# Kernel tuning notes

Hardware: AMD Instinct MI355X
Metric: run time of the kernel (lower is better)

The kernel has to match this reference:

```python
import jax, jax.numpy as jnp
import numpy as np

N, E, F, H, C = 50000, 800000, 128, 256, 40
BN_EPS = 1e-5


def setup_inputs() -> dict:
    key = jax.random.key(0)
    ks = jax.random.split(key, 18)

    def lin(kw, kb, fan_in, fan_out):
        s = 1.0 / np.sqrt(fan_in)
        W = jax.random.uniform(kw, (fan_in, fan_out), minval=-s, maxval=s, dtype=jnp.float32)
        b = jax.random.uniform(kb, (fan_out,), minval=-s, maxval=s, dtype=jnp.float32)
        return W, b

    x = jax.random.normal(ks[0], (N, F), dtype=jnp.float32)
    edge_index = jax.random.randint(ks[1], (2, E), 0, N, dtype=jnp.int32)
    edge_weight = jax.random.uniform(ks[2], (E,), dtype=jnp.float32)

    W_edge, b_edge = lin(ks[3], ks[4], N, H)   # SparseLinear: weight [num_nodes, H]
    W_node, b_node = lin(ks[5], ks[6], F, H)   # node_mlp (single layer)
    W_c1, b_c1 = lin(ks[7], ks[8], H, H)       # cat_lin1
    W_c2, b_c2 = lin(ks[9], ks[10], H, H)      # cat_lin2
    W_f1, b_f1 = lin(ks[11], ks[12], H, H)     # final_mlp layer 1
    W_f2, b_f2 = lin(ks[13], ks[14], H, C)     # final_mlp layer 2 (plain last)
    gamma = jnp.ones((H,), jnp.float32)        # BatchNorm1d weight
    beta = jnp.zeros((H,), jnp.float32)        # BatchNorm1d bias

    return {"x": x, "edge_index": edge_index, "edge_weight": edge_weight,
            "W_edge": W_edge, "b_edge": b_edge, "W_node": W_node, "b_node": b_node,
            "W_c1": W_c1, "b_c1": b_c1, "W_c2": W_c2, "b_c2": b_c2,
            "W_f1": W_f1, "b_f1": b_f1, "gamma": gamma, "beta": beta,
            "W_f2": W_f2, "b_f2": b_f2}


def reference(x, edge_index, edge_weight, W_edge, b_edge, W_node, b_node,
              W_c1, b_c1, W_c2, b_c2, W_f1, b_f1, gamma, beta, W_f2, b_f2):
    src, dst = edge_index[0], edge_index[1]
    # SparseLinear: gather weight rows at sources, scale by edge weight, scatter-add at targets
    msgs = edge_weight[:, None] * W_edge[src]                 # [E, H]
    h_a = jax.ops.segment_sum(msgs, dst, num_segments=W_edge.shape[0]) + b_edge  # [N, H]

    out = h_a + (h_a @ W_c1 + b_c1)
    h_x = x @ W_node + b_node                                  # node_mlp (plain linear)
    out = out + h_x + (h_x @ W_c2 + b_c2)
    out = jax.nn.relu(out)

    # final_mlp: Linear -> ReLU (act_first) -> BatchNorm (training stats) -> Linear
    h = jax.nn.relu(out @ W_f1 + b_f1)
    mu = jnp.mean(h, axis=0)
    var = jnp.mean(jnp.square(h - mu), axis=0)                 # biased var, as torch BN
    h = (h - mu) * jax.lax.rsqrt(var + BN_EPS) * gamma + beta
    return h @ W_f2 + b_f2                                     # [N, C]
```

## Files before the change

### kernel.cpp

```cpp
#include <hip/hip_runtime.h>

#define NN 50000
#define EE 800000
#define FF 128
#define HH 256
#define CC 40
#define BN_EPS 1e-5f
#define NBUCK 196
#define CHK 3200
#define BCAP 6144

typedef float f4 __attribute__((ext_vector_type(4)));
typedef float f2 __attribute__((ext_vector_type(2)));
typedef _Float16 h8 __attribute__((ext_vector_type(8)));
typedef _Float16 h4 __attribute__((ext_vector_type(4)));

#define OFF_NODE 0
#define OFF_C1   32768
#define OFF_F1   98304
#define PW_HALVES 163840

#define SWZ(row, c2) ((c2) ^ (((row) & 7) << 4))

__global__ __launch_bounds__(256)
void k_wcomb(const float* __restrict__ Wn, const float* __restrict__ Wc2,
             float* __restrict__ Wcomb, int* __restrict__ btail,
             float* __restrict__ stats) {
    if (blockIdx.x == 8) {
        if (threadIdx.x < NBUCK) btail[threadIdx.x] = threadIdx.x * BCAP;
        stats[threadIdx.x] = 0.f;
        stats[256 + threadIdx.x] = 0.f;
        return;
    }
    __shared__ float WnL[16][256];
    const int c = threadIdx.x;
    const int r0 = blockIdx.x * 16;
    for (int i = threadIdx.x; i < 16 * 256; i += 256)
        WnL[i >> 8][i & 255] = Wn[(r0 + (i >> 8)) * HH + (i & 255)];
    __syncthreads();
    float acc[16];
#pragma unroll
    for (int r = 0; r < 16; ++r) acc[r] = WnL[r][c];
    for (int k = 0; k < 256; ++k) {
        float wv = Wc2[k * HH + c];
#pragma unroll
        for (int r = 0; r < 16; ++r) acc[r] += WnL[r][k] * wv;
    }
#pragma unroll
    for (int r = 0; r < 16; ++r) Wcomb[(r0 + r) * HH + c] = acc[r];
}

__global__ __launch_bounds__(256)
void k_prep(const float* __restrict__ W, unsigned char* __restrict__ W8,
            const float* __restrict__ x, _Float16* __restrict__ x16) {
    const int gsz = gridDim.x * blockDim.x;
    const int i0 = blockIdx.x * blockDim.x + threadIdx.x;
    for (int j = i0; j < NN * HH / 8; j += gsz) {
        f4 v0 = ((const f4*)W)[j * 2];
        f4 v1 = ((const f4*)W)[j * 2 + 1];
        int p0 = 0, p1 = 0;
        p0 = __builtin_amdgcn_cvt_pk_fp8_f32(v0[0] * 256.f, v0[1] * 256.f, p0, false);
        p0 = __builtin_amdgcn_cvt_pk_fp8_f32(v0[2] * 256.f, v0[3] * 256.f, p0, true);
        p1 = __builtin_amdgcn_cvt_pk_fp8_f32(v1[0] * 256.f, v1[1] * 256.f, p1, false);
        p1 = __builtin_amdgcn_cvt_pk_fp8_f32(v1[2] * 256.f, v1[3] * 256.f, p1, true);
        uint2 u;
        u.x = (unsigned int)p0;
        u.y = (unsigned int)p1;
        ((uint2*)W8)[j] = u;
    }
    for (int j = i0; j < NN * FF / 8; j += gsz) {
        f4 v0 = ((const f4*)x)[j * 2];
        f4 v1 = ((const f4*)x)[j * 2 + 1];
        h8 h;
        h[0] = (_Float16)v0[0]; h[1] = (_Float16)v0[1];
        h[2] = (_Float16)v0[2]; h[3] = (_Float16)v0[3];
        h[4] = (_Float16)v1[0]; h[5] = (_Float16)v1[1];
        h[6] = (_Float16)v1[2]; h[7] = (_Float16)v1[3];
        ((h8*)x16)[j] = h;
    }
}

__global__ __launch_bounds__(256)
void k_pack(const float* __restrict__ Wcomb, const float* __restrict__ W_c1,
            const float* __restrict__ W_c2, const float* __restrict__ W_f1,
            const float* __restrict__ b_node, const float* __restrict__ b_c1,
            const float* __restrict__ b_c2, _Float16* __restrict__ pW,
            float* __restrict__ bB) {
    const int tid = threadIdx.x;
    if (blockIdx.x == 80) {
        int c = tid;
        if (c < HH) {
            float a = 0.f;
            for (int k = 0; k < HH; ++k) a += b_node[k] * W_c2[k * HH + c];
            bB[c] = a + b_node[c] + b_c1[c] + b_c2[c];
        }
        return;
    }
    const int unit = blockIdx.x * 4 + (tid >> 6);
    const int lane = tid & 63, lm = lane & 15, lg = lane >> 4;
    const float* Ws;
    bool addI;
    int u = unit;
    if (u < 64)       { Ws = Wcomb; addI = false; }
    else if (u < 192) { Ws = W_c1;  addI = true;  u -= 64; }
    else              { Ws = W_f1;  addI = false; u -= 192; }
    const int kb = u >> 4, nb = u & 15;
    h8 hv;
#pragma unroll
    for (int j = 0; j < 8; ++j) {
        int kr = kb * 32 + lg * 8 + j;
        int col = nb * 16 + lm;
        float v = Ws[kr * HH + col];
        if (addI && kr == col) v += 1.f;
        hv[j] = (_Float16)v;
    }
    *(h8*)(pW + (size_t)unit * 512 + lane * 8) = hv;
}

__global__ __launch_bounds__(256)
void k_binA(const int* __restrict__ ei, const float* __restrict__ ew,
            int* __restrict__ btail, uint2* __restrict__ tmp) {
    __shared__ int lcnt[NBUCK], lpre[NBUCK], lbase[NBUCK], lcnt2[NBUCK];
    __shared__ int t[256];
    __shared__ uint2 staged[CHK];
    __shared__ unsigned char bslot[CHK];
    const int tid = threadIdx.x;
    const int e0 = blockIdx.x * CHK;
    const int n = min(CHK, EE - e0);
    for (int i = tid; i < NBUCK; i += 256) { lcnt[i] = 0; lcnt2[i] = 0; }
    __syncthreads();
    for (int i = tid; i < n; i += 256) {
        int d = ei[EE + e0 + i];
        atomicAdd(&lcnt[d >> 8], 1);
    }
    __syncthreads();
    {
        int v = (tid < NBUCK) ? lcnt[tid] : 0;
        t[tid] = v;
        __syncthreads();
#pragma unroll
        for (int off = 1; off < 256; off <<= 1) {
            int u = (tid >= off) ? t[tid - off] : 0;
            __syncthreads();
            t[tid] += u;
            __syncthreads();
        }
        if (tid < NBUCK) lpre[tid] = t[tid] - v;
    }
    __syncthreads();
    if (tid < NBUCK && lcnt[tid] > 0)
        lbase[tid] = atomicAdd(&btail[tid], lcnt[tid]);
    __syncthreads();
    for (int i = tid; i < n; i += 256) {
        int e = e0 + i;
        int d = ei[EE + e];
        int b = d >> 8;
        _Float16 hw = (_Float16)ew[e];
        unsigned short hwb = *(unsigned short*)&hw;
        unsigned int lo = (unsigned int)ei[e] | ((unsigned int)hwb << 16);
        int slot = lpre[b] + atomicAdd(&lcnt2[b], 1);
        uint2 v;
        v.x = lo;
        v.y = (unsigned int)d;
        staged[slot] = v;
        bslot[slot] = (unsigned char)b;
    }
    __syncthreads();
    for (int s = tid; s < n; s += 256) {
        int b = bslot[s];
        int idx = lbase[b] + (s - lpre[b]);
        if (idx < (b + 1) * BCAP) tmp[idx] = staged[s];
    }
}

__global__ __launch_bounds__(256)
void k_binB(const int* __restrict__ btail, const uint2* __restrict__ tmp,
            unsigned int* __restrict__ esw, int* __restrict__ rowptr) {
    __shared__ int lpos[256], lpre[256];
    __shared__ int t[256];
    __shared__ unsigned int sout[BCAP];
    const int tid = threadIdx.x;
    const int b = blockIdx.x;
    const int nb0 = b * 256;
    const int tb = b * BCAP;
    const int cnt = btail[b] - tb;
    t[tid] = (tid < b) ? (btail[tid] - tid * BCAP) : 0;
    __syncthreads();
#pragma unroll
    for (int off = 128; off > 0; off >>= 1) {
        if (tid < off) t[tid] += t[tid + off];
        __syncthreads();
    }
    const int gbase = t[0];
    __syncthreads();
    lpos[tid] = 0;
    __syncthreads();
    for (int i = tid; i < cnt; i += 256)
        atomicAdd(&lpos[(int)tmp[tb + i].y - nb0], 1);
    __syncthreads();
    {
        int v = lpos[tid];
        t[tid] = v;
        __syncthreads();
#pragma unroll
        for (int off = 1; off < 256; off <<= 1) {
            int u = (tid >= off) ? t[tid - off] : 0;
            __syncthreads();
            t[tid] += u;
            __syncthreads();
        }
        lpre[tid] = t[tid] - v;
    }
    __syncthreads();
    if (nb0 + tid < NN) rowptr[nb0 + tid] = gbase + lpre[tid];
    if (b == NBUCK - 1 && tid == 0) rowptr[NN] = EE;
    lpos[tid] = lpre[tid];
    __syncthreads();
    for (int i = tid; i < cnt; i += 256) {
        uint2 v = tmp[tb + i];
        int dr = (int)v.y - nb0;
        int p = atomicAdd(&lpos[dr], 1);
        sout[p] = v.x;
    }
    __syncthreads();
    for (int s = tid; s < cnt; s += 256) esw[gbase + s] = sout[s];
}

__global__ __launch_bounds__(256)
void k_gather(const int* __restrict__ rowptr, const unsigned int* __restrict__ esw,
              const unsigned char* __restrict__ W8, const float* __restrict__ b_edge,
              _Float16* __restrict__ outHA) {
    const int wave = threadIdx.x >> 6;
    const int lane = threadIdx.x & 63;
    const int node = blockIdx.x * 4 + wave;
    if (node >= NN) return;
    int e = rowptr[node];
    const int end = rowptr[node + 1];
    const int c0 = lane * 4;
    f4 acc0 = {0.f, 0.f, 0.f, 0.f}, acc1 = {0.f, 0.f, 0.f, 0.f};
    for (; e + 7 < end; e += 8) {
        unsigned int v[8];
        unsigned int rw[8];
#pragma unroll
        for (int j = 0; j < 8; ++j) v[j] = esw[e + j];
#pragma unroll
        for (int j = 0; j < 8; ++j)
            rw[j] = *(const unsigned int*)(W8 + (size_t)(v[j] & 0xFFFF) * HH + c0);
#pragma unroll
        for (int j = 0; j < 8; j += 2) {
            unsigned short b0 = (unsigned short)(v[j] >> 16);
            unsigned short b1 = (unsigned short)(v[j + 1] >> 16);
            float w0 = (float)*(_Float16*)&b0;
            float w1 = (float)*(_Float16*)&b1;
            f2 l0 = __builtin_amdgcn_cvt_pk_f32_fp8((int)rw[j], false);
            f2 h0 = __builtin_amdgcn_cvt_pk_f32_fp8((int)rw[j], true);
            f2 l1 = __builtin_amdgcn_cvt_pk_f32_fp8((int)rw[j + 1], false);
            f2 h1 = __builtin_amdgcn_cvt_pk_f32_fp8((int)rw[j + 1], true);
            f4 f0 = {l0[0], l0[1], h0[0], h0[1]};
            f4 f1 = {l1[0], l1[1], h1[0], h1[1]};
            acc0 += w0 * f0;
            acc1 += w1 * f1;
        }
    }
    if (e < end) {
        const int rem = end - e;
        unsigned int v[8];
        unsigned int rw[8];
#pragma unroll
        for (int j = 0; j < 8; ++j) v[j] = esw[(j < rem) ? (e + j) : e];
#pragma unroll
        for (int j = 0; j < 8; ++j)
            rw[j] = *(const unsigned int*)(W8 + (size_t)(v[j] & 0xFFFF) * HH + c0);
#pragma unroll
        for (int j = 0; j < 8; j += 2) {
            unsigned short b0 = (unsigned short)(v[j] >> 16);
            unsigned short b1 = (unsigned short)(v[j + 1] >> 16);
            float w0 = (j < rem) ? (float)*(_Float16*)&b0 : 0.f;
            float w1 = (j + 1 < rem) ? (float)*(_Float16*)&b1 : 0.f;
            f2 l0 = __builtin_amdgcn_cvt_pk_f32_fp8((int)rw[j], false);
            f2 h0 = __builtin_amdgcn_cvt_pk_f32_fp8((int)rw[j], true);
            f2 l1 = __builtin_amdgcn_cvt_pk_f32_fp8((int)rw[j + 1], false);
            f2 h1 = __builtin_amdgcn_cvt_pk_f32_fp8((int)rw[j + 1], true);
            f4 f0 = {l0[0], l0[1], h0[0], h0[1]};
            f4 f1 = {l1[0], l1[1], h1[0], h1[1]};
            acc0 += w0 * f0;
            acc1 += w1 * f1;
        }
    }
    f4 b = *(const f4*)(b_edge + c0);
    f4 acc = (acc0 + acc1) * (1.f / 256.f) + b;
    h4 hv;
    hv[0] = (_Float16)acc[0]; hv[1] = (_Float16)acc[1];
    hv[2] = (_Float16)acc[2]; hv[3] = (_Float16)acc[3];
    *(h4*)(outHA + (size_t)node * HH + c0) = hv;
}

__global__ __launch_bounds__(512)
void k_gemmBC(const _Float16* __restrict__ x16, const _Float16* __restrict__ A1,
              const _Float16* __restrict__ pW, const float* __restrict__ bB,
              const float* __restrict__ b_f1, _Float16* __restrict__ H,
              float* __restrict__ stats) {
    __shared__ __align__(16) char sm[40960];
    const int tid = threadIdx.x;
    const int w = tid >> 6, l = tid & 63;
    const int lm = l & 15, lg = l >> 4;

    h8 w1[8][2], wc[4][2], wf[8][2];
#pragma unroll
    for (int kb = 0; kb < 8; ++kb)
#pragma unroll
        for (int n = 0; n < 2; ++n) {
            w1[kb][n] = *(const h8*)(pW + OFF_C1 + (size_t)(kb * 16 + w * 2 + n) * 512 + l * 8);
            wf[kb][n] = *(const h8*)(pW + OFF_F1 + (size_t)(kb * 16 + w * 2 + n) * 512 + l * 8);
        }
#pragma unroll
    for (int kb = 0; kb < 4; ++kb)
#pragma unroll
        for (int n = 0; n < 2; ++n)
            wc[kb][n] = *(const h8*)(pW + OFF_NODE + (size_t)(kb * 16 + w * 2 + n) * 512 + l * 8);

    float bBreg[2], bFreg[2];
#pragma unroll
    for (int n = 0; n < 2; ++n) {
        bBreg[n] = bB[w * 32 + n * 16 + lm];
        bFreg[n] = b_f1[w * 32 + n * 16 + lm];
    }
    float sS[2] = {0.f, 0.f}, sQ[2] = {0.f, 0.f};

    const int NT = (NN + 31) / 32;
    int4 pX;
    int4 p1[2];
    int t = blockIdx.x;
    {
        const int rX = tid >> 4, sX_ = tid & 15;
        int grow = t * 32 + rX;
        int4 z = {0, 0, 0, 0};
        pX = (grow < NN) ? *(const int4*)(x16 + (size_t)grow * FF + sX_ * 8) : z;
#pragma unroll
        for (int j = 0; j < 2; ++j) {
            int unit = tid * 2 + j;
            int r = unit >> 5, s = unit & 31;
            int g2 = t * 32 + r;
            p1[j] = (g2 < NN) ? *(const int4*)(A1 + (size_t)g2 * HH + s * 8) : z;
        }
    }

    for (; t < NT; t += gridDim.x) {
        {
            const int rX = tid >> 4, sX_ = tid & 15;
            *(int4*)(sm + rX * 256 + SWZ(rX, sX_ * 16)) = pX;
        }
#pragma unroll
        for (int j = 0; j < 2; ++j) {
            int unit = tid * 2 + j;
            int r = unit >> 5, s = unit & 31;
            *(int4*)(sm + 8192 + r * 512 + SWZ(r, s * 16)) = p1[j];
        }
        int tn = t + gridDim.x;
        if (tn < NT) {
            const int rX = tid >> 4, sX_ = tid & 15;
            int grow = tn * 32 + rX;
            int4 z = {0, 0, 0, 0};
            pX = (grow < NN) ? *(const int4*)(x16 + (size_t)grow * FF + sX_ * 8) : z;
#pragma unroll
            for (int j = 0; j < 2; ++j) {
                int unit = tid * 2 + j;
                int r = unit >> 5, s = unit & 31;
                int g2 = tn * 32 + r;
                p1[j] = (g2 < NN) ? *(const int4*)(A1 + (size_t)g2 * HH + s * 8) : z;
            }
        }
        __syncthreads();

        f4 acc[2][2];
        const f4 z4 = {0.f, 0.f, 0.f, 0.f};
#pragma unroll
        for (int rf = 0; rf < 2; ++rf)
#pragma unroll
            for (int n = 0; n < 2; ++n) acc[rf][n] = z4;

#pragma unroll
        for (int kb = 0; kb < 8; ++kb) {
            h8 a0 = *(const h8*)(sm + 8192 + lm * 512 + SWZ(lm, kb * 64 + lg * 16));
            h8 a1 = *(const h8*)(sm + 8192 + (16 + lm) * 512 + SWZ(16 + lm, kb * 64 + lg * 16));
#pragma unroll
            for (int n = 0; n < 2; ++n) {
                acc[0][n] = __builtin_amdgcn_mfma_f32_16x16x32_f16(a0, w1[kb][n], acc[0][n], 0, 0, 0);
                acc[1][n] = __builtin_amdgcn_mfma_f32_16x16x32_f16(a1, w1[kb][n], acc[1][n], 0, 0, 0);
            }
        }
#pragma unroll
        for (int kb = 0; kb < 4; ++kb) {
            h8 a0 = *(const h8*)(sm + lm * 256 + SWZ(lm, kb * 64 + lg * 16));
            h8 a1 = *(const h8*)(sm + (16 + lm) * 256 + SWZ(16 + lm, kb * 64 + lg * 16));
#pragma unroll
            for (int n = 0; n < 2; ++n) {
                acc[0][n] = __builtin_amdgcn_mfma_f32_16x16x32_f16(a0, wc[kb][n], acc[0][n], 0, 0, 0);
                acc[1][n] = __builtin_amdgcn_mfma_f32_16x16x32_f16(a1, wc[kb][n], acc[1][n], 0, 0, 0);
            }
        }
#pragma unroll
        for (int rf = 0; rf < 2; ++rf)
#pragma unroll
            for (int n = 0; n < 2; ++n) {
                int c2 = (w * 32 + n * 16 + lm) * 2;
#pragma unroll
                for (int q = 0; q < 4; ++q) {
                    int r = rf * 16 + lg * 4 + q;
                    float v = fmaxf(acc[rf][n][q] + bBreg[n], 0.f);
                    *(_Float16*)(sm + 24576 + r * 512 + SWZ(r, c2)) = (_Float16)v;
                }
            }
        __syncthreads();

#pragma unroll
        for (int rf = 0; rf < 2; ++rf)
#pragma unroll
            for (int n = 0; n < 2; ++n) acc[rf][n] = z4;

#pragma unroll
        for (int kb = 0; kb < 8; ++kb) {
            h8 a0 = *(const h8*)(sm + 24576 + lm * 512 + SWZ(lm, kb * 64 + lg * 16));
            h8 a1 = *(const h8*)(sm + 24576 + (16 + lm) * 512 + SWZ(16 + lm, kb * 64 + lg * 16));
#pragma unroll
            for (int n = 0; n < 2; ++n) {
                acc[0][n] = __builtin_amdgcn_mfma_f32_16x16x32_f16(a0, wf[kb][n], acc[0][n], 0, 0, 0);
                acc[1][n] = __builtin_amdgcn_mfma_f32_16x16x32_f16(a1, wf[kb][n], acc[1][n], 0, 0, 0);
            }
        }

        const int row0 = t * 32;
#pragma unroll
        for (int rf = 0; rf < 2; ++rf)
#pragma unroll
            for (int n = 0; n < 2; ++n) {
                const int col = w * 32 + n * 16 + lm;
#pragma unroll
                for (int q = 0; q < 4; ++q) {
                    int grow = row0 + rf * 16 + lg * 4 + q;
                    if (grow < NN) {
                        float v = fmaxf(acc[rf][n][q] + bFreg[n], 0.f);
                        sS[n] += v;
                        sQ[n] += v * v;
                        H[(size_t)grow * HH + col] = (_Float16)v;
                    }
                }
            }
        __syncthreads();
    }

#pragma unroll
    for (int n = 0; n < 2; ++n) {
        float s = sS[n];
        s += __shfl_xor(s, 16); s += __shfl_xor(s, 32);
        float q = sQ[n];
        q += __shfl_xor(q, 16); q += __shfl_xor(q, 32);
        if (lg == 0) {
            atomicAdd(&stats[w * 32 + n * 16 + lm], s);
            atomicAdd(&stats[HH + w * 32 + n * 16 + lm], q);
        }
    }
}

__global__ __launch_bounds__(256)
void k_bnprep(const float* __restrict__ stats, const float* __restrict__ gamma,
              const float* __restrict__ beta, const float* __restrict__ W_f2,
              const float* __restrict__ b_f2, _Float16* __restrict__ pWf,
              float* __restrict__ bfold) {
    __shared__ float sh[HH];
    __shared__ float ssc[HH];
    const int tid = threadIdx.x;
    const float invN = 1.0f / (float)NN;
    {
        float mu = stats[tid] * invN;
        float var = stats[HH + tid] * invN - mu * mu;
        float scale = gamma[tid] * rsqrtf(var + BN_EPS);
        sh[tid] = beta[tid] - mu * scale;
        ssc[tid] = scale;
    }
    __syncthreads();
    if (tid < CC) {
        float b = b_f2[tid];
        for (int k = 0; k < HH; ++k) b += sh[k] * W_f2[k * CC + tid];
        bfold[tid] = b;
    }
    const int w = tid >> 6, l = tid & 63;
    const int lm = l & 15, lg = l >> 4;
#pragma unroll
    for (int i = 0; i < 6; ++i) {
        int u = w + i * 4;
        int kb = u / 3, nb = u % 3;
        h8 hv;
#pragma unroll
        for (int j = 0; j < 8; ++j) {
            int k = kb * 32 + lg * 8 + j;
            int c = nb * 16 + lm;
            float v = (c < CC) ? ssc[k] * W_f2[k * CC + c] : 0.f;
            hv[j] = (_Float16)v;
        }
        *(h8*)(pWf + (size_t)u * 512 + l * 8) = hv;
    }
}

__global__ __launch_bounds__(256)
void k_finalM(const _Float16* __restrict__ h, const _Float16* __restrict__ pWf,
              const float* __restrict__ bfold, float* __restrict__ out) {
    __shared__ __align__(16) char sA[64 * 512];
    const int tid = threadIdx.x;
    const int w = tid >> 6, l = tid & 63;
    const int lm = l & 15, lg = l >> 4;

    h8 wreg[8][3];
#pragma unroll
    for (int kb = 0; kb < 8; ++kb)
#pragma unroll
        for (int nb = 0; nb < 3; ++nb)
            wreg[kb][nb] = *(const h8*)(pWf + (size_t)(kb * 3 + nb) * 512 + l * 8);

    const int row0 = blockIdx.x * 64;
#pragma unroll
    for (int j = 0; j < 8; ++j) {
        int unit = tid * 8 + j;
        int r = unit >> 5, s = unit & 31;
        int grow = row0 + r;
        int4 z = {0, 0, 0, 0};
        int4 v = (grow < NN) ? *(const int4*)(h + (size_t)grow * HH + s * 8) : z;
        *(int4*)(sA + r * 512 + SWZ(r, s * 16)) = v;
    }
    __syncthreads();

    f4 acc[3];
    const f4 z4 = {0.f, 0.f, 0.f, 0.f};
#pragma unroll
    for (int nb = 0; nb < 3; ++nb) acc[nb] = z4;

    const int ar = w * 16 + lm;
#pragma unroll
    for (int kb = 0; kb < 8; ++kb) {
        h8 a = *(const h8*)(sA + ar * 512 + SWZ(ar, kb * 64 + lg * 16));
#pragma unroll
        for (int nb = 0; nb < 3; ++nb)
            acc[nb] = __builtin_amdgcn_mfma_f32_16x16x32_f16(a, wreg[kb][nb], acc[nb], 0, 0, 0);
    }

#pragma unroll
    for (int nb = 0; nb < 3; ++nb) {
        int col = nb * 16 + lm;
        if (col < CC) {
            float bb = bfold[col];
#pragma unroll
            for (int q = 0; q < 4; ++q) {
                int grow = row0 + w * 16 + lg * 4 + q;
                if (grow < NN) out[(size_t)grow * CC + col] = acc[nb][q] + bb;
            }
        }
    }
}

extern "C" void kernel_launch(void* const* d_in, const int* in_sizes, int n_in,
                              void* d_out, int out_size, void* d_ws, size_t ws_size,
                              hipStream_t stream) {
    const float* x      = (const float*)d_in[0];
    const int*   ei     = (const int*)d_in[1];
    const float* ew     = (const float*)d_in[2];
    const float* W_edge = (const float*)d_in[3];
    const float* b_edge = (const float*)d_in[4];
    const float* W_node = (const float*)d_in[5];
    const float* b_node = (const float*)d_in[6];
    const float* W_c1   = (const float*)d_in[7];
    const float* b_c1   = (const float*)d_in[8];
    const float* W_c2   = (const float*)d_in[9];
    const float* b_c2   = (const float*)d_in[10];
    const float* W_f1   = (const float*)d_in[11];
    const float* b_f1   = (const float*)d_in[12];
    const float* gamma  = (const float*)d_in[13];
    const float* beta   = (const float*)d_in[14];
    const float* W_f2   = (const float*)d_in[15];
    const float* b_f2   = (const float*)d_in[16];
    float* out = (float*)d_out;

    const size_t NNH = (size_t)NN * HH;
    _Float16* bufA = (_Float16*)d_ws;
    _Float16* bufH = bufA + NNH;
    _Float16* x16  = bufH + NNH;
    unsigned char* W8 = (unsigned char*)(x16 + (size_t)NN * FF);
    unsigned int* esw = (unsigned int*)(W8 + NNH);
    float* stats   = (float*)(esw + EE);
    float* bB      = stats + 2 * HH;
    float* bfold   = bB + HH;
    _Float16* pWf  = (_Float16*)(bfold + 64);
    _Float16* pW   = pWf + 24 * 512;
    float* Wcomb   = (float*)(pW + PW_HALVES);
    uint2* tmp     = (uint2*)(Wcomb + FF * HH);
    int* rowptr    = (int*)(tmp + (size_t)NBUCK * BCAP);
    int* btail     = rowptr + NN + 1;

    k_wcomb<<<9, 256, 0, stream>>>(W_node, W_c2, Wcomb, btail, stats);
    k_prep<<<2048, 256, 0, stream>>>(W_edge, W8, x, x16);
    k_pack<<<81, 256, 0, stream>>>(Wcomb, W_c1, W_c2, W_f1, b_node, b_c1, b_c2, pW, bB);
    k_binA<<<(EE + CHK - 1) / CHK, 256, 0, stream>>>(ei, ew, btail, tmp);
    k_binB<<<NBUCK, 256, 0, stream>>>(btail, tmp, esw, rowptr);
    k_gather<<<12500, 256, 0, stream>>>(rowptr, esw, W8, b_edge, bufA);

    k_gemmBC<<<256, 512, 0, stream>>>(x16, bufA, pW, bB, b_f1, bufH, stats);

    k_bnprep<<<1, 256, 0, stream>>>(stats, gamma, beta, W_f2, b_f2, pWf, bfold);
    k_finalM<<<(NN + 63) / 64, 256, 0, stream>>>(bufH, pWf, bfold, out);
}
```

Baseline: 179.7 us.

## Load MFMA A-operands directly from global memory and double the gemm grid

Removes the register-prefetch and LDS staging of the x16 and A1 tiles in the fused gemm kernel. Each lane now reads its MFMA A fragments straight from global memory, clamping row indices at the tail. LDS drops to the 16 KB output tile and the grid grows from 256 to 512 blocks to raise occupancy. The cost is that every wave in the block re-reads the same A rows from global/L2, and the software prefetch that overlapped the next tile's loads is gone.

```diff
diff --git a/kernel.cpp b/kernel.cpp
--- a/kernel.cpp
+++ b/kernel.cpp
@@ -300,7 +300,7 @@
               const _Float16* __restrict__ pW, const float* __restrict__ bB,
               const float* __restrict__ b_f1, _Float16* __restrict__ H,
               float* __restrict__ stats) {
-    __shared__ __align__(16) char sm[40960];
+    __shared__ __align__(16) char sOut[32 * 512];
     const int tid = threadIdx.x;
     const int w = tid >> 6, l = tid & 63;
     const int lm = l & 15, lg = l >> 4;
@@ -328,52 +328,13 @@
     float sS[2] = {0.f, 0.f}, sQ[2] = {0.f, 0.f};
 
     const int NT = (NN + 31) / 32;
-    int4 pX;
-    int4 p1[2];
-    int t = blockIdx.x;
-    {
-        const int rX = tid >> 4, sX_ = tid & 15;
-        int grow = t * 32 + rX;
-        int4 z = {0, 0, 0, 0};
-        pX = (grow < NN) ? *(const int4*)(x16 + (size_t)grow * FF + sX_ * 8) : z;
-#pragma unroll
-        for (int j = 0; j < 2; ++j) {
-            int unit = tid * 2 + j;
-            int r = unit >> 5, s = unit & 31;
-            int g2 = t * 32 + r;
-            p1[j] = (g2 < NN) ? *(const int4*)(A1 + (size_t)g2 * HH + s * 8) : z;
-        }
-    }
-
-    for (; t < NT; t += gridDim.x) {
-        {
-            const int rX = tid >> 4, sX_ = tid & 15;
-            *(int4*)(sm + rX * 256 + SWZ(rX, sX_ * 16)) = pX;
-        }
-#pragma unroll
-        for (int j = 0; j < 2; ++j) {
-            int unit = tid * 2 + j;
-            int r = unit >> 5, s = unit & 31;
-            *(int4*)(sm + 8192 + r * 512 + SWZ(r, s * 16)) = p1[j];
-        }
-        int tn = t + gridDim.x;
-        if (tn < NT) {
-            const int rX = tid >> 4, sX_ = tid & 15;
-            int grow = tn * 32 + rX;
-            int4 z = {0, 0, 0, 0};
-            pX = (grow < NN) ? *(const int4*)(x16 + (size_t)grow * FF + sX_ * 8) : z;
-#pragma unroll
-            for (int j = 0; j < 2; ++j) {
-                int unit = tid * 2 + j;
-                int r = unit >> 5, s = unit & 31;
-                int g2 = tn * 32 + r;
-                p1[j] = (g2 < NN) ? *(const int4*)(A1 + (size_t)g2 * HH + s * 8) : z;
-            }
-        }
-        __syncthreads();
+    const f4 z4 = {0.f, 0.f, 0.f, 0.f};
+
+    for (int t = blockIdx.x; t < NT; t += gridDim.x) {
+        const int r0 = min(t * 32 + lm, NN - 1);
+        const int r1 = min(t * 32 + 16 + lm, NN - 1);
 
         f4 acc[2][2];
-        const f4 z4 = {0.f, 0.f, 0.f, 0.f};
 #pragma unroll
         for (int rf = 0; rf < 2; ++rf)
 #pragma unroll
@@ -381,8 +342,8 @@
 
 #pragma unroll
         for (int kb = 0; kb < 8; ++kb) {
-            h8 a0 = *(const h8*)(sm + 8192 + lm * 512 + SWZ(lm, kb * 64 + lg * 16));
-            h8 a1 = *(const h8*)(sm + 8192 + (16 + lm) * 512 + SWZ(16 + lm, kb * 64 + lg * 16));
+            h8 a0 = *(const h8*)(A1 + (size_t)r0 * HH + kb * 32 + lg * 8);
+            h8 a1 = *(const h8*)(A1 + (size_t)r1 * HH + kb * 32 + lg * 8);
 #pragma unroll
             for (int n = 0; n < 2; ++n) {
                 acc[0][n] = __builtin_amdgcn_mfma_f32_16x16x32_f16(a0, w1[kb][n], acc[0][n], 0, 0, 0);
@@ -391,8 +352,8 @@
         }
 #pragma unroll
         for (int kb = 0; kb < 4; ++kb) {
-            h8 a0 = *(const h8*)(sm + lm * 256 + SWZ(lm, kb * 64 + lg * 16));
-            h8 a1 = *(const h8*)(sm + (16 + lm) * 256 + SWZ(16 + lm, kb * 64 + lg * 16));
+            h8 a0 = *(const h8*)(x16 + (size_t)r0 * FF + kb * 32 + lg * 8);
+            h8 a1 = *(const h8*)(x16 + (size_t)r1 * FF + kb * 32 + lg * 8);
 #pragma unroll
             for (int n = 0; n < 2; ++n) {
                 acc[0][n] = __builtin_amdgcn_mfma_f32_16x16x32_f16(a0, wc[kb][n], acc[0][n], 0, 0, 0);
@@ -408,7 +369,7 @@
                 for (int q = 0; q < 4; ++q) {
                     int r = rf * 16 + lg * 4 + q;
                     float v = fmaxf(acc[rf][n][q] + bBreg[n], 0.f);
-                    *(_Float16*)(sm + 24576 + r * 512 + SWZ(r, c2)) = (_Float16)v;
+                    *(_Float16*)(sOut + r * 512 + SWZ(r, c2)) = (_Float16)v;
                 }
             }
         __syncthreads();
@@ -420,8 +381,8 @@
 
 #pragma unroll
         for (int kb = 0; kb < 8; ++kb) {
-            h8 a0 = *(const h8*)(sm + 24576 + lm * 512 + SWZ(lm, kb * 64 + lg * 16));
-            h8 a1 = *(const h8*)(sm + 24576 + (16 + lm) * 512 + SWZ(16 + lm, kb * 64 + lg * 16));
+            h8 a0 = *(const h8*)(sOut + lm * 512 + SWZ(lm, kb * 64 + lg * 16));
+            h8 a1 = *(const h8*)(sOut + (16 + lm) * 512 + SWZ(16 + lm, kb * 64 + lg * 16));
 #pragma unroll
             for (int n = 0; n < 2; ++n) {
                 acc[0][n] = __builtin_amdgcn_mfma_f32_16x16x32_f16(a0, wf[kb][n], acc[0][n], 0, 0, 0);
@@ -602,7 +563,7 @@
     k_binB<<<NBUCK, 256, 0, stream>>>(btail, tmp, esw, rowptr);
     k_gather<<<12500, 256, 0, stream>>>(rowptr, esw, W8, b_edge, bufA);
 
-    k_gemmBC<<<256, 512, 0, stream>>>(x16, bufA, pW, bB, b_f1, bufH, stats);
+    k_gemmBC<<<512, 512, 0, stream>>>(x16, bufA, pW, bB, b_f1, bufH, stats);
 
     k_bnprep<<<1, 256, 0, stream>>>(stats, gamma, beta, W_f2, b_f2, pWf, bfold);
     k_finalM<<<(NN + 63) / 64, 256, 0, stream>>>(bufH, pWf, bfold, out);
```

New measurement: 206.8 us. 1.15x slower.
